# Kernel tuning notes

Measured on AMD Instinct MI355X. Metric: run time of the kernel, lower is better.

The kernel has to match this reference:

```python
import jax, jax.numpy as jnp
import numpy as np

B, T, IDIM, ODIM, HDIM, CDIM = 8, 8192, 256, 256, 1024, 128


def setup_inputs() -> dict:
    key = jax.random.key(0)
    ks = jax.random.split(key, 7)
    s_enc = 1.0 / np.sqrt(IDIM)
    s_dec = 1.0 / np.sqrt(HDIM)
    return {
        "x": jax.random.normal(ks[0], (B, T, IDIM), jnp.float32),
        "mask_prev": jnp.zeros((B, T, HDIM), jnp.float32),
        "W_enc": jax.random.uniform(ks[1], (IDIM, HDIM), jnp.float32, -s_enc, s_enc),
        "b_enc": jax.random.uniform(ks[2], (HDIM,), jnp.float32, -s_enc, s_enc),
        "W_dec_self": jax.random.uniform(ks[3], (HDIM, IDIM), jnp.float32, -s_dec, s_dec),
        "b_dec_self": jax.random.uniform(ks[4], (IDIM,), jnp.float32, -s_dec, s_dec),
        "W_dec_src": jax.random.uniform(ks[5], (HDIM, ODIM), jnp.float32, -s_dec, s_dec),
        "b_dec_src": jax.random.uniform(ks[6], (ODIM,), jnp.float32, -s_dec, s_dec),
        "decoder_type": 0,  # 0 = 'self', 1 = 'src'
    }


def _topk_masks(h, cdim):
    # energy_pooling_mask with share=True: topk(k=2*cdim) of h^2 along hdim.
    energy = h * h  # [B,T,H]
    _, idx = jax.lax.top_k(energy, 2 * cdim)  # [B,T,2C] indices into H
    bi = jnp.arange(h.shape[0])[:, None, None]
    ti = jnp.arange(h.shape[1])[None, :, None]
    # scatter instead of materializing one_hot [B,T,2C,H]
    mask = jnp.zeros_like(h).at[bi, ti, idx[..., :cdim]].add(1.0)
    mask_share = jnp.zeros_like(h).at[bi, ti, idx].add(1.0)
    return mask, mask_share


def reference(x, mask_prev, W_enc, b_enc, W_dec_self, b_dec_self, W_dec_src, b_dec_src, decoder_type):
    # encoder
    h = jnp.einsum("bti,ih->bth", x, W_enc) + b_enc  # [B,T,H]
    # hidden_exclude_activation (mask_prev provided): zero previously-used units
    h = jnp.where(mask_prev > 0, 0.0, h)
    mask_cur, mask_cur_share = _topk_masks(h, CDIM)
    mask_new = mask_prev + mask_cur
    h = jnp.where(mask_cur_share > 0, h, 0.0)
    # decoder (idim == odim asserted in original)
    if decoder_type == 0:
        out = jnp.einsum("bth,ho->bto", h, W_dec_self) + b_dec_self
    else:
        out = jnp.einsum("bth,ho->bto", h, W_dec_src) + b_dec_src
    return out, mask_new
```

## Files before the change

### kernel.cpp

```cpp
#include <hip/hip_runtime.h>
#include <hip/hip_bf16.h>

#define B_ 8
#define T_ 8192
#define M_ (B_ * T_)
#define IDIM 256
#define HDIM 1024
#define ODIM 256
#define CDIM 128
#define OUT_OFF ((size_t)M_ * ODIM)

typedef __attribute__((ext_vector_type(4))) float floatx4;
typedef __attribute__((ext_vector_type(8))) short shortx8;

__global__ __launch_bounds__(256) void k0_convw(const float* __restrict__ Wself,
                                                const float* __restrict__ Wsrc,
                                                const int* __restrict__ dtype,
                                                __hip_bfloat16* __restrict__ WdT) {
    int id = blockIdx.x * 256 + threadIdx.x;
    int n = id >> 10;
    int k = id & 1023;
    const float* W = (*dtype == 0) ? Wself : Wsrc;
    WdT[id] = __float2bfloat16(W[(size_t)k * ODIM + n]);
}

__global__ __launch_bounds__(256) void k1_enc(const float* __restrict__ X,
                                              const float* __restrict__ W,
                                              const float* __restrict__ bias,
                                              float* __restrict__ H) {
    __shared__ __align__(16) float As[32][132];
    __shared__ __align__(16) float Bs[32][128];
    const int t  = threadIdx.x;
    const int m0 = blockIdx.x * 128;
    const int n0 = blockIdx.y * 128;
    const int tx = t & 15;
    const int ty = t >> 4;

    int arow[4], ak4[4], brow[4], bc4[4];
#pragma unroll
    for (int r = 0; r < 4; ++r) {
        int idx = t + r * 256;
        arow[r] = idx >> 3;
        ak4[r]  = (idx & 7) << 2;
        brow[r] = idx >> 5;
        bc4[r]  = (idx & 31) << 2;
    }

    float acc[8][8];
#pragma unroll
    for (int i = 0; i < 8; ++i)
#pragma unroll
        for (int j = 0; j < 8; ++j) acc[i][j] = 0.0f;

    float4 apre[4], bpre[4];
#pragma unroll
    for (int r = 0; r < 4; ++r) {
        apre[r] = *(const float4*)(X + (size_t)(m0 + arow[r]) * IDIM + ak4[r]);
        bpre[r] = *(const float4*)(W + (size_t)brow[r] * HDIM + n0 + bc4[r]);
    }
#pragma unroll
    for (int r = 0; r < 4; ++r) {
        As[ak4[r] + 0][arow[r]] = apre[r].x;
        As[ak4[r] + 1][arow[r]] = apre[r].y;
        As[ak4[r] + 2][arow[r]] = apre[r].z;
        As[ak4[r] + 3][arow[r]] = apre[r].w;
        *(float4*)&Bs[brow[r]][bc4[r]] = bpre[r];
    }
    __syncthreads();

#pragma unroll 1
    for (int kt = 0; kt < 8; ++kt) {
        if (kt < 7) {
            int kn = (kt + 1) * 32;
#pragma unroll
            for (int r = 0; r < 4; ++r) {
                apre[r] = *(const float4*)(X + (size_t)(m0 + arow[r]) * IDIM + kn + ak4[r]);
                bpre[r] = *(const float4*)(W + (size_t)(kn + brow[r]) * HDIM + n0 + bc4[r]);
            }
        }
#pragma unroll 8
        for (int k = 0; k < 32; ++k) {
            float4 a0 = *(const float4*)&As[k][ty * 8];
            float4 a1 = *(const float4*)&As[k][ty * 8 + 4];
            float4 b0 = *(const float4*)&Bs[k][tx * 4];
            float4 b1 = *(const float4*)&Bs[k][tx * 4 + 64];
            float av[8] = {a0.x, a0.y, a0.z, a0.w, a1.x, a1.y, a1.z, a1.w};
            float bv[8] = {b0.x, b0.y, b0.z, b0.w, b1.x, b1.y, b1.z, b1.w};
#pragma unroll
            for (int i = 0; i < 8; ++i)
#pragma unroll
                for (int j = 0; j < 8; ++j)
                    acc[i][j] = fmaf(av[i], bv[j], acc[i][j]);
        }
        __syncthreads();
        if (kt < 7) {
#pragma unroll
            for (int r = 0; r < 4; ++r) {
                As[ak4[r] + 0][arow[r]] = apre[r].x;
                As[ak4[r] + 1][arow[r]] = apre[r].y;
                As[ak4[r] + 2][arow[r]] = apre[r].z;
                As[ak4[r] + 3][arow[r]] = apre[r].w;
                *(float4*)&Bs[brow[r]][bc4[r]] = bpre[r];
            }
            __syncthreads();
        }
    }

#pragma unroll
    for (int i = 0; i < 8; ++i) {
        int gm = m0 + ty * 8 + i;
        float* o = H + (size_t)gm * HDIM + n0;
        float4 v0, v1;
        v0.x = acc[i][0] + bias[n0 + tx * 4 + 0];
        v0.y = acc[i][1] + bias[n0 + tx * 4 + 1];
        v0.z = acc[i][2] + bias[n0 + tx * 4 + 2];
        v0.w = acc[i][3] + bias[n0 + tx * 4 + 3];
        v1.x = acc[i][4] + bias[n0 + 64 + tx * 4 + 0];
        v1.y = acc[i][5] + bias[n0 + 64 + tx * 4 + 1];
        v1.z = acc[i][6] + bias[n0 + 64 + tx * 4 + 2];
        v1.w = acc[i][7] + bias[n0 + 64 + tx * 4 + 3];
        *(float4*)(o + tx * 4) = v0;
        *(float4*)(o + 64 + tx * 4) = v1;
    }
}

#define NBIN 512
#define KBASE 1600
#define CAP 128

__device__ __forceinline__ unsigned int bsearch_kth(const unsigned int* u, int k,
                                                    int lane, int* r_out) {
    unsigned long long lo = 0, hi = 0xFFFFFFFFull;
    while (lo < hi) {
        unsigned int mid = (unsigned int)((lo + hi + 1) >> 1);
        int c = 0;
#pragma unroll
        for (int i = 0; i < 16; ++i) c += (u[i] >= mid) ? 1 : 0;
#pragma unroll
        for (int off = 1; off < 64; off <<= 1) {
            int o = __shfl_down(c, off, 64);
            if (lane + off < 64) c += o;
        }
        c = __shfl(c, 0);
        if (c >= k) lo = mid; else hi = (unsigned long long)mid - 1;
    }
    unsigned int T = (unsigned int)lo;
    int g = 0;
#pragma unroll
    for (int i = 0; i < 16; ++i) g += (u[i] > T) ? 1 : 0;
#pragma unroll
    for (int off = 1; off < 64; off <<= 1) {
        int o = __shfl_down(g, off, 64);
        if (lane + off < 64) g += o;
    }
    g = __shfl(g, 0);
    *r_out = k - g;
    return T;
}

__global__ __launch_bounds__(256) void k2_topk(const float* __restrict__ mask_prev,
                                               float* __restrict__ Hio,
                                               __hip_bfloat16* __restrict__ Abf) {
    __shared__ unsigned int hist[4][NBIN];
    __shared__ unsigned long long cand[4][2][CAP];
    __shared__ unsigned int sres[4][8];
    __shared__ unsigned int scnt[4][2];
    const int t = threadIdx.x;
    const int wave = t >> 6;
    const int lane = t & 63;
    const size_t row = (size_t)blockIdx.x * 4 + wave;
    const float* mp = mask_prev + row * HDIM;
    float* hrow = Hio + row * HDIM;

    float hv[16], mpv[16];
    unsigned int u[16];
    int bin[16];
#pragma unroll
    for (int i = 0; i < 16; ++i) {
        int j = lane + (i << 6);
        float m = mp[j];
        float h = hrow[j];
        h = (m > 0.0f) ? 0.0f : h;
        mpv[i] = m; hv[i] = h;
        float e = h * h;
        u[i] = __float_as_uint(e);
        int b = (int)(u[i] >> 19) - KBASE;
        bin[i] = (b < 0) ? 0 : ((b > NBIN - 1) ? NBIN - 1 : b);
    }

#pragma unroll
    for (int q = 0; q < 8; ++q) hist[wave][lane + (q << 6)] = 0u;
    if (lane < 2) scnt[wave][lane] = 0u;
    __syncthreads();
#pragma unroll
    for (int i = 0; i < 16; ++i) atomicAdd(&hist[wave][bin[i]], 1u);
    __syncthreads();

    {
        unsigned int cj[8]; unsigned int lt = 0;
#pragma unroll
        for (int jj = 0; jj < 8; ++jj) { cj[jj] = hist[wave][lane * 8 + jj]; lt += cj[jj]; }
        unsigned int s = lt;
#pragma unroll
        for (int off = 1; off < 64; off <<= 1) {
            unsigned int o = (unsigned int)__shfl_down((int)s, off, 64);
            if (lane + off < 64) s += o;
        }
        unsigned int run = s - lt;
#pragma unroll
        for (int jj = 7; jj >= 0; --jj) {
            unsigned int gt = run, ge = run + cj[jj];
            if (gt < CDIM && CDIM <= ge)         { sres[wave][0] = lane * 8 + jj; sres[wave][1] = CDIM - gt; }
            if (gt < 2 * CDIM && 2 * CDIM <= ge) { sres[wave][2] = lane * 8 + jj; sres[wave][3] = 2 * CDIM - gt; }
            run = ge;
        }
    }
    __syncthreads();
    const unsigned int b1 = sres[wave][0], kk1 = sres[wave][1];
    const unsigned int b2 = sres[wave][2], kk2 = sres[wave][3];

#pragma unroll
    for (int i = 0; i < 16; ++i) {
        int j = lane + (i << 6);
        unsigned long long pk = ((unsigned long long)u[i] << 32) | (unsigned int)(1023 - j);
        if ((unsigned int)bin[i] == b1) {
            unsigned int p = atomicAdd(&scnt[wave][0], 1u);
            if (p < CAP) cand[wave][0][p] = pk;
        }
        if (b2 != b1 && (unsigned int)bin[i] == b2) {
            unsigned int p = atomicAdd(&scnt[wave][1], 1u);
            if (p < CAP) cand[wave][1][p] = pk;
        }
    }
    __syncthreads();
    const unsigned int C1 = scnt[wave][0];
    const unsigned int C2 = (b2 == b1) ? C1 : scnt[wave][1];
    const unsigned long long* L2 = (b2 == b1) ? cand[wave][0] : cand[wave][1];

    if (C1 <= CAP) {
        for (unsigned int idx = lane; idx < C1; idx += 64) {
            unsigned long long mine = cand[wave][0][idx];
            unsigned int myu = (unsigned int)(mine >> 32);
            unsigned int rank = 0, gtu = 0;
            for (unsigned int c = 0; c < C1; ++c) {
                unsigned long long o = cand[wave][0][c];
                rank += (o > mine) ? 1u : 0u;
                gtu  += ((unsigned int)(o >> 32) > myu) ? 1u : 0u;
            }
            if (rank == kk1 - 1) { sres[wave][4] = myu; sres[wave][5] = gtu; }
        }
    }
    if (C2 <= CAP) {
        for (unsigned int idx = lane; idx < C2; idx += 64) {
            unsigned long long mine = L2[idx];
            unsigned int myu = (unsigned int)(mine >> 32);
            unsigned int rank = 0, gtu = 0;
            for (unsigned int c = 0; c < C2; ++c) {
                unsigned long long o = L2[c];
                rank += (o > mine) ? 1u : 0u;
                gtu  += ((unsigned int)(o >> 32) > myu) ? 1u : 0u;
            }
            if (rank == kk2 - 1) { sres[wave][6] = myu; sres[wave][7] = gtu; }
        }
    }
    __syncthreads();

    unsigned int T1, T2; int r1, r2;
    if (C1 <= CAP) { T1 = sres[wave][4]; r1 = (int)(kk1 - sres[wave][5]); }
    else           { T1 = bsearch_kth(u, CDIM, lane, &r1); }
    if (C2 <= CAP) { T2 = sres[wave][6]; r2 = (int)(kk2 - sres[wave][7]); }
    else           { T2 = bsearch_kth(u, 2 * CDIM, lane, &r2); }

    const unsigned long long below = (1ULL << lane) - 1ULL;
    int c1 = 0, c2 = 0;
#pragma unroll
    for (int i = 0; i < 16; ++i) {
        unsigned long long bb1 = __ballot(u[i] == T1);
        unsigned long long bb2 = __ballot(u[i] == T2);
        bool s1 = (u[i] > T1) || ((u[i] == T1) && (c1 + (int)__popcll(bb1 & below) < r1));
        bool s2 = (u[i] > T2) || ((u[i] == T2) && (c2 + (int)__popcll(bb2 & below) < r2));
        c1 += (int)__popcll(bb1);
        c2 += (int)__popcll(bb2);
        int j = lane + (i << 6);
        hrow[j] = mpv[i] + (s1 ? 1.0f : 0.0f);
        Abf[row * HDIM + j] = __float2bfloat16(s2 ? hv[i] : 0.0f);
    }
}

#define K3LD 40
__global__ __launch_bounds__(256) void k3_dec(const __hip_bfloat16* __restrict__ A,
                                              const __hip_bfloat16* __restrict__ Bt,
                                              const float* __restrict__ bias_self,
                                              const float* __restrict__ bias_src,
                                              const int* __restrict__ dtype,
                                              float* __restrict__ Out) {
    __shared__ __align__(16) __hip_bfloat16 As[128 * K3LD];
    __shared__ __align__(16) __hip_bfloat16 Bs[128 * K3LD];
    const int t = threadIdx.x;
    const int lane = t & 63;
    const int wave = t >> 6;
    const int m0 = blockIdx.x * 128;
    const int n0 = blockIdx.y * 128;
    const int wr = wave >> 1;
    const int wc = wave & 1;
    const int quad = lane >> 4;
    const int rf = lane & 15;

    int srow[2], skc[2];
#pragma unroll
    for (int p = 0; p < 2; ++p) {
        int l = p * 256 + t;
        srow[p] = l >> 2;
        skc[p]  = (l & 3) << 3;
    }

    floatx4 acc[4][4];
    const floatx4 z = {0.0f, 0.0f, 0.0f, 0.0f};
#pragma unroll
    for (int i = 0; i < 4; ++i)
#pragma unroll
        for (int j = 0; j < 4; ++j) acc[i][j] = z;

    uint4 apre[2], bpre[2];
#pragma unroll
    for (int p = 0; p < 2; ++p) {
        apre[p] = *(const uint4*)(A  + (size_t)(m0 + srow[p]) * HDIM + skc[p]);
        bpre[p] = *(const uint4*)(Bt + (size_t)(n0 + srow[p]) * HDIM + skc[p]);
    }
#pragma unroll
    for (int p = 0; p < 2; ++p) {
        *(uint4*)&As[srow[p] * K3LD + skc[p]] = apre[p];
        *(uint4*)&Bs[srow[p] * K3LD + skc[p]] = bpre[p];
    }
    __syncthreads();

#pragma unroll 1
    for (int kt = 0; kt < HDIM / 32; ++kt) {
        if (kt < HDIM / 32 - 1) {
            int kn = (kt + 1) * 32;
#pragma unroll
            for (int p = 0; p < 2; ++p) {
                apre[p] = *(const uint4*)(A  + (size_t)(m0 + srow[p]) * HDIM + kn + skc[p]);
                bpre[p] = *(const uint4*)(Bt + (size_t)(n0 + srow[p]) * HDIM + kn + skc[p]);
            }
        }
        shortx8 af[4], bf[4];
#pragma unroll
        for (int i = 0; i < 4; ++i) {
            af[i] = *(const shortx8*)&As[(wr * 64 + i * 16 + rf) * K3LD + quad * 8];
            bf[i] = *(const shortx8*)&Bs[(wc * 64 + i * 16 + rf) * K3LD + quad * 8];
        }
#pragma unroll
        for (int mi = 0; mi < 4; ++mi)
#pragma unroll
            for (int nj = 0; nj < 4; ++nj)
                acc[mi][nj] = __builtin_amdgcn_mfma_f32_16x16x32_bf16(
                    af[mi], bf[nj], acc[mi][nj], 0, 0, 0);
        __syncthreads();
        if (kt < HDIM / 32 - 1) {
#pragma unroll
            for (int p = 0; p < 2; ++p) {
                *(uint4*)&As[srow[p] * K3LD + skc[p]] = apre[p];
                *(uint4*)&Bs[srow[p] * K3LD + skc[p]] = bpre[p];
            }
            __syncthreads();
        }
    }

    const float* bias = (*dtype == 0) ? bias_self : bias_src;
#pragma unroll
    for (int mi = 0; mi < 4; ++mi) {
#pragma unroll
        for (int nj = 0; nj < 4; ++nj) {
            int gn = n0 + wc * 64 + nj * 16 + rf;
            float bv = bias[gn];
            int gmb = m0 + wr * 64 + mi * 16 + quad * 4;
#pragma unroll
            for (int r2 = 0; r2 < 4; ++r2)
                Out[(size_t)(gmb + r2) * ODIM + gn] = acc[mi][nj][r2] + bv;
        }
    }
}

extern "C" void kernel_launch(void* const* d_in, const int* in_sizes, int n_in,
                              void* d_out, int out_size, void* d_ws, size_t ws_size,
                              hipStream_t stream) {
    const float* x          = (const float*)d_in[0];
    const float* mask_prev  = (const float*)d_in[1];
    const float* W_enc      = (const float*)d_in[2];
    const float* b_enc      = (const float*)d_in[3];
    const float* W_dec_self = (const float*)d_in[4];
    const float* b_dec_self = (const float*)d_in[5];
    const float* W_dec_src  = (const float*)d_in[6];
    const float* b_dec_src  = (const float*)d_in[7];
    const int*   dtype      = (const int*)d_in[8];

    float* out  = (float*)d_out;
    float* Hbuf = out + OUT_OFF;

    __hip_bfloat16* Abf = (__hip_bfloat16*)d_ws;
    __hip_bfloat16* WdT = (__hip_bfloat16*)((char*)d_ws + (size_t)M_ * HDIM * 2);

    k0_convw<<<dim3((ODIM * HDIM) / 256), 256, 0, stream>>>(W_dec_self, W_dec_src, dtype, WdT);
    k1_enc  <<<dim3(M_ / 128, HDIM / 128), 256, 0, stream>>>(x, W_enc, b_enc, Hbuf);
    k2_topk <<<dim3(M_ / 4), 256, 0, stream>>>(mask_prev, Hbuf, Abf);
    k3_dec  <<<dim3(M_ / 128, ODIM / 128), 256, 0, stream>>>(Abf, WdT, b_dec_self, b_dec_src, dtype, out);
}
```

Measured before the change: 1.187 ms.

## Vectorize top-k row I/O with contiguous lane chunks and drop encoder prefetch

The top-k kernel now gives each lane 16 contiguous elements instead of strided ones. This allows float4 loads of mask_prev and h, float4 stores of the new mask, and 16-byte packed bf16 stores. Tie-break ordering moves from per-element ballots to a per-lane count followed by a wave-wide prefix scan over shuffles, so tie order still follows index order. Separately, the encoder GEMM drops its register-prefetch double buffering in favour of a simpler load-sync-compute loop, which may expose global load latency but frees registers.

```diff
diff --git a/kernel.cpp b/kernel.cpp
--- a/kernel.cpp
+++ b/kernel.cpp
@@ -36,48 +36,34 @@
     const int tx = t & 15;
     const int ty = t >> 4;
 
-    int arow[4], ak4[4], brow[4], bc4[4];
-#pragma unroll
-    for (int r = 0; r < 4; ++r) {
-        int idx = t + r * 256;
-        arow[r] = idx >> 3;
-        ak4[r]  = (idx & 7) << 2;
-        brow[r] = idx >> 5;
-        bc4[r]  = (idx & 31) << 2;
-    }
-
     float acc[8][8];
 #pragma unroll
     for (int i = 0; i < 8; ++i)
 #pragma unroll
         for (int j = 0; j < 8; ++j) acc[i][j] = 0.0f;
 
-    float4 apre[4], bpre[4];
-#pragma unroll
-    for (int r = 0; r < 4; ++r) {
-        apre[r] = *(const float4*)(X + (size_t)(m0 + arow[r]) * IDIM + ak4[r]);
-        bpre[r] = *(const float4*)(W + (size_t)brow[r] * HDIM + n0 + bc4[r]);
-    }
-#pragma unroll
-    for (int r = 0; r < 4; ++r) {
-        As[ak4[r] + 0][arow[r]] = apre[r].x;
-        As[ak4[r] + 1][arow[r]] = apre[r].y;
-        As[ak4[r] + 2][arow[r]] = apre[r].z;
-        As[ak4[r] + 3][arow[r]] = apre[r].w;
-        *(float4*)&Bs[brow[r]][bc4[r]] = bpre[r];
-    }
-    __syncthreads();
-
-#pragma unroll 1
-    for (int kt = 0; kt < 8; ++kt) {
-        if (kt < 7) {
-            int kn = (kt + 1) * 32;
-#pragma unroll
-            for (int r = 0; r < 4; ++r) {
-                apre[r] = *(const float4*)(X + (size_t)(m0 + arow[r]) * IDIM + kn + ak4[r]);
-                bpre[r] = *(const float4*)(W + (size_t)(kn + brow[r]) * HDIM + n0 + bc4[r]);
-            }
-        }
+    for (int kk = 0; kk < IDIM; kk += 32) {
+#pragma unroll
+        for (int r = 0; r < 4; ++r) {
+            int idx = t + r * 256;
+            int row = idx >> 3;
+            int k4  = (idx & 7) << 2;
+            float4 a = *(const float4*)(X + (size_t)(m0 + row) * IDIM + kk + k4);
+            As[k4 + 0][row] = a.x;
+            As[k4 + 1][row] = a.y;
+            As[k4 + 2][row] = a.z;
+            As[k4 + 3][row] = a.w;
+        }
+#pragma unroll
+        for (int r = 0; r < 4; ++r) {
+            int idx = t + r * 256;
+            int row = idx >> 5;
+            int c4  = (idx & 31) << 2;
+            *(float4*)&Bs[row][c4] =
+                *(const float4*)(W + (size_t)(kk + row) * HDIM + n0 + c4);
+        }
+        __syncthreads();
+
 #pragma unroll 8
         for (int k = 0; k < 32; ++k) {
             float4 a0 = *(const float4*)&As[k][ty * 8];
@@ -93,17 +79,6 @@
                     acc[i][j] = fmaf(av[i], bv[j], acc[i][j]);
         }
         __syncthreads();
-        if (kt < 7) {
-#pragma unroll
-            for (int r = 0; r < 4; ++r) {
-                As[ak4[r] + 0][arow[r]] = apre[r].x;
-                As[ak4[r] + 1][arow[r]] = apre[r].y;
-                As[ak4[r] + 2][arow[r]] = apre[r].z;
-                As[ak4[r] + 3][arow[r]] = apre[r].w;
-                *(float4*)&Bs[brow[r]][bc4[r]] = bpre[r];
-            }
-            __syncthreads();
-        }
     }
 
 #pragma unroll
@@ -169,23 +144,27 @@
     const int wave = t >> 6;
     const int lane = t & 63;
     const size_t row = (size_t)blockIdx.x * 4 + wave;
-    const float* mp = mask_prev + row * HDIM;
-    float* hrow = Hio + row * HDIM;
+    const float* mp = mask_prev + row * HDIM + lane * 16;
+    float* hrow = Hio + row * HDIM + lane * 16;
 
     float hv[16], mpv[16];
     unsigned int u[16];
     int bin[16];
 #pragma unroll
-    for (int i = 0; i < 16; ++i) {
-        int j = lane + (i << 6);
-        float m = mp[j];
-        float h = hrow[j];
-        h = (m > 0.0f) ? 0.0f : h;
-        mpv[i] = m; hv[i] = h;
-        float e = h * h;
-        u[i] = __float_as_uint(e);
-        int b = (int)(u[i] >> 19) - KBASE;
-        bin[i] = (b < 0) ? 0 : ((b > NBIN - 1) ? NBIN - 1 : b);
+    for (int c = 0; c < 4; ++c) {
+        float4 m4 = *(const float4*)(mp + c * 4);
+        float4 h4 = *(const float4*)(hrow + c * 4);
+        float mm[4] = {m4.x, m4.y, m4.z, m4.w};
+        float hh[4] = {h4.x, h4.y, h4.z, h4.w};
+#pragma unroll
+        for (int x = 0; x < 4; ++x) {
+            int i = c * 4 + x;
+            float h = (mm[x] > 0.0f) ? 0.0f : hh[x];
+            mpv[i] = mm[x]; hv[i] = h;
+            u[i] = __float_as_uint(h * h);
+            int b = (int)(u[i] >> 19) - KBASE;
+            bin[i] = (b < 0) ? 0 : ((b > NBIN - 1) ? NBIN - 1 : b);
+        }
     }
 
 #pragma unroll
@@ -221,7 +200,7 @@
 
 #pragma unroll
     for (int i = 0; i < 16; ++i) {
-        int j = lane + (i << 6);
+        int j = lane * 16 + i;
         unsigned long long pk = ((unsigned long long)u[i] << 32) | (unsigned int)(1023 - j);
         if ((unsigned int)bin[i] == b1) {
             unsigned int p = atomicAdd(&scnt[wave][0], 1u);
@@ -271,19 +250,48 @@
     if (C2 <= CAP) { T2 = sres[wave][6]; r2 = (int)(kk2 - sres[wave][7]); }
     else           { T2 = bsearch_kth(u, 2 * CDIM, lane, &r2); }
 
-    const unsigned long long below = (1ULL << lane) - 1ULL;
-    int c1 = 0, c2 = 0;
+    int p1[16], p2[16];
+    int tot1 = 0, tot2 = 0;
 #pragma unroll
     for (int i = 0; i < 16; ++i) {
-        unsigned long long bb1 = __ballot(u[i] == T1);
-        unsigned long long bb2 = __ballot(u[i] == T2);
-        bool s1 = (u[i] > T1) || ((u[i] == T1) && (c1 + (int)__popcll(bb1 & below) < r1));
-        bool s2 = (u[i] > T2) || ((u[i] == T2) && (c2 + (int)__popcll(bb2 & below) < r2));
-        c1 += (int)__popcll(bb1);
-        c2 += (int)__popcll(bb2);
-        int j = lane + (i << 6);
-        hrow[j] = mpv[i] + (s1 ? 1.0f : 0.0f);
-        Abf[row * HDIM + j] = __float2bfloat16(s2 ? hv[i] : 0.0f);
+        p1[i] = tot1; p2[i] = tot2;
+        tot1 += (u[i] == T1) ? 1 : 0;
+        tot2 += (u[i] == T2) ? 1 : 0;
+    }
+    int s1v = tot1, s2v = tot2;
+#pragma unroll
+    for (int off = 1; off < 64; off <<= 1) {
+        int o1 = __shfl_up(s1v, off, 64);
+        int o2 = __shfl_up(s2v, off, 64);
+        if (lane >= off) { s1v += o1; s2v += o2; }
+    }
+    const int ex1 = s1v - tot1;
+    const int ex2 = s2v - tot2;
+
+#pragma unroll
+    for (int c = 0; c < 4; ++c) {
+        float v[4];
+#pragma unroll
+        for (int x = 0; x < 4; ++x) {
+            int i = c * 4 + x;
+            bool s1 = (u[i] > T1) || ((u[i] == T1) && (ex1 + p1[i] < r1));
+            v[x] = mpv[i] + (s1 ? 1.0f : 0.0f);
+        }
+        float4 v4 = {v[0], v[1], v[2], v[3]};
+        *(float4*)(hrow + c * 4) = v4;
+    }
+    __hip_bfloat16* ab = Abf + row * HDIM + lane * 16;
+#pragma unroll
+    for (int half = 0; half < 2; ++half) {
+        union { unsigned short us[8]; uint4 v; } pk;
+#pragma unroll
+        for (int x = 0; x < 8; ++x) {
+            int i = half * 8 + x;
+            bool s2 = (u[i] > T2) || ((u[i] == T2) && (ex2 + p2[i] < r2));
+            __hip_bfloat16 bb = __float2bfloat16(s2 ? hv[i] : 0.0f);
+            pk.us[x] = *(unsigned short*)&bb;
+        }
+        *(uint4*)(ab + half * 8) = pk.v;
     }
 }
 
```

New measurement: 1.163 ms. -2.0%, faster.
